# Optimization experiments

Hardware: AMD Instinct MI355X
Metric: run time of the kernel (lower is better)

The kernel has to match this reference:

```python
import jax, jax.numpy as jnp
import numpy as np

NUM_EXPERTS = 8
TOPK = 2
HIDDEN = 2048
INTER = 1024          # intermediate_size_per_rank (world_size = 1)
NTOKENS = 8192        # ntokens; rows of intermediate_states = NTOKENS * TOPK


def setup_inputs() -> dict:
    key = jax.random.key(0)
    k1, k2, k3 = jax.random.split(key, 3)
    intermediate_states = jax.random.normal(k1, (NTOKENS * TOPK, INTER), jnp.float32) * 0.02
    w = jax.random.normal(k2, (NUM_EXPERTS, INTER, HIDDEN), jnp.float32) * 0.02
    router_logits = jax.random.normal(k3, (NTOKENS, NUM_EXPERTS), jnp.float32)
    return {"intermediate_states": intermediate_states, "w": w, "router_logits": router_logits}


def reference(intermediate_states, w, router_logits):
    # select_experts: softmax over experts, then top-k (ids + weights)
    probs = jax.nn.softmax(router_logits, axis=-1)              # [T, E]
    topk_weight, topk_ids = jax.lax.top_k(probs, TOPK)          # [T, K]
    tw = topk_weight.reshape(-1)                                # [T*K]
    tids = topk_ids.reshape(-1)                                 # [T*K]

    # per-expert masked GEMM + router-weight scale (expert loop is a small fixed set)
    out = jnp.zeros((NTOKENS * TOPK, HIDDEN), intermediate_states.dtype)
    for e in range(NUM_EXPERTS):
        mask = (tids == e)[:, None]                             # [T*K, 1]
        xe = jnp.where(mask, intermediate_states, 0.0)          # gather via masking
        out = out + jnp.where(mask, (xe @ w[e]) * tw[:, None], 0.0)

    # sum over topk; reduce_scatter with world_size==1 is the identity
    output = out.reshape(NTOKENS, TOPK, HIDDEN).sum(axis=1)     # [T, H]
    return output
```

## Files before the change

### kernel.cpp

```cpp
#include <hip/hip_runtime.h>
#include <hip/hip_bf16.h>

#define NTOK   8192
#define TOPK   2
#define NROWS  (NTOK*TOPK)
#define NEXP   8
#define KDIM   1024
#define NDIM   2048
#define TM     128
#define TN     128
#define BK     64
#define MAXYT  136
#define NXT    (NDIM/TN)
#define GRID_G (MAXYT*NXT)

typedef __bf16 bf16_t;
typedef __bf16 bf16x8 __attribute__((ext_vector_type(8)));
typedef float  f32x4  __attribute__((ext_vector_type(4)));

static_assert(sizeof(bf16x8) == 16, "bf16x8 must be 16B");

#define OFF_TW    ((size_t)0)
#define OFF_INV   ((size_t)(1<<16))
#define OFF_CNT   ((size_t)(1<<17))
#define OFF_RL    ((size_t)(1<<18))
#define OFF_XP    ((size_t)(1<<20))
#define OFF_WB    ((size_t)(34u<<20))
#define OFF_SCR   ((size_t)(68u<<20))

__device__ __forceinline__ void gload_lds16(const bf16_t* g, const char* l) {
  __builtin_amdgcn_global_load_lds(
      (const __attribute__((address_space(1))) void*)g,
      (__attribute__((address_space(3))) void*)(void*)l, 16, 0, 0);
}

#define CVT8(lo,hi) bf16x8{ (bf16_t)(lo).x,(bf16_t)(lo).y,(bf16_t)(lo).z,(bf16_t)(lo).w, \
                            (bf16_t)(hi).x,(bf16_t)(hi).y,(bf16_t)(hi).z,(bf16_t)(hi).w }

__global__ void routing_kernel(const float* __restrict__ logits,
                               float* __restrict__ tw,
                               int* __restrict__ cnt, int* __restrict__ rowlist) {
  __shared__ int lcnt[NEXP];
  __shared__ int lbase[NEXP];
  int tid = threadIdx.x;
  int t = blockIdx.x * blockDim.x + tid;
  if (tid < NEXP) lcnt[tid] = 0;
  __syncthreads();

  float4 a = *(const float4*)(logits + (size_t)t*NEXP);
  float4 b = *(const float4*)(logits + (size_t)t*NEXP + 4);
  float l[8] = {a.x, a.y, a.z, a.w, b.x, b.y, b.z, b.w};
  float m = l[0];
#pragma unroll
  for (int i = 1; i < 8; i++) m = fmaxf(m, l[i]);
  float p[8], s = 0.f;
#pragma unroll
  for (int i = 0; i < 8; i++) { p[i] = __expf(l[i] - m); s += p[i]; }
  int e0 = 0; float b0 = p[0];
#pragma unroll
  for (int i = 1; i < 8; i++) if (p[i] > b0) { b0 = p[i]; e0 = i; }
  int e1 = (e0 == 0) ? 1 : 0; float b1 = p[e1];
#pragma unroll
  for (int i = 0; i < 8; i++) if (i != e0 && p[i] > b1) { b1 = p[i]; e1 = i; }
  float inv = 1.f / s;
  tw[2*t]   = b0 * inv;
  tw[2*t+1] = b1 * inv;

  int lp0 = atomicAdd(&lcnt[e0], 1);
  int lp1 = atomicAdd(&lcnt[e1], 1);
  __syncthreads();
  if (tid < NEXP) lbase[tid] = atomicAdd(&cnt[tid], lcnt[tid]);
  __syncthreads();
  rowlist[(size_t)e0*NROWS + lbase[e0] + lp0] = 2*t;
  rowlist[(size_t)e1*NROWS + lbase[e1] + lp1] = 2*t + 1;
}

__global__ void cvt_kernel(const float* __restrict__ x,
                           const int* __restrict__ cnt,
                           const int* __restrict__ rowlist,
                           bf16_t* __restrict__ xp,
                           int* __restrict__ inv,
                           const float* __restrict__ w,
                           bf16_t* __restrict__ wb) {
  __shared__ float tf[64*65];
  int bid = blockIdx.x;
  int tid = threadIdx.x;

  if (bid < 2048) {
    int rid = bid * 8 + (tid >> 6);
    int c   = (tid & 63) * 16;
    int e = 0, base = 0, acc = 0;
#pragma unroll
    for (int ee = 0; ee < NEXP; ee++) {
      int ce = cnt[ee];
      if (rid >= acc && rid < acc + ce) { e = ee; base = acc; }
      acc += ce;
    }
    int src = rowlist[(size_t)e*NROWS + (rid - base)];
    const float* sp = x + (size_t)src*KDIM + c;
    float4 v0 = *(const float4*)(sp);
    float4 v1 = *(const float4*)(sp + 4);
    float4 v2 = *(const float4*)(sp + 8);
    float4 v3 = *(const float4*)(sp + 12);
    bf16_t* dp = xp + (size_t)rid*KDIM + c;
    *(bf16x8*)(dp)     = CVT8(v0, v1);
    *(bf16x8*)(dp + 8) = CVT8(v2, v3);
    if ((tid & 63) == 0) inv[src] = rid;
    return;
  }

  int id = bid - 2048;
  int e  = id >> 9;
  int k0 = ((id >> 5) & 15) * 64;
  int n0 = (id & 31) * 64;
  const float* src = w + (size_t)e*KDIM*NDIM + (size_t)k0*NDIM + n0;
#pragma unroll
  for (int i = 0; i < 2; i++) {
    int idx = tid + i*512;
    int kr  = idx >> 4;
    int nc4 = (idx & 15) * 4;
    float4 v = *(const float4*)(src + (size_t)kr*NDIM + nc4);
    tf[kr*65 + nc4+0] = v.x; tf[kr*65 + nc4+1] = v.y;
    tf[kr*65 + nc4+2] = v.z; tf[kr*65 + nc4+3] = v.w;
  }
  __syncthreads();
  bf16_t* dst = wb + (size_t)e*NDIM*KDIM + (size_t)n0*KDIM + k0;
  {
    int idx = tid;
    int nr  = idx >> 3;
    int kc  = (idx & 7) * 8;
    bf16x8 o;
#pragma unroll
    for (int j = 0; j < 8; j++) o[j] = (bf16_t)tf[(kc+j)*65 + nr];
    *(bf16x8*)(dst + (size_t)nr*KDIM + kc) = o;
  }
}

__global__ __launch_bounds__(256)
void gemm_kernel(const bf16_t* __restrict__ xp,
                 const bf16_t* __restrict__ wb,
                 const int*    __restrict__ cnt,
                 bf16_t*       __restrict__ scrb) {
  __shared__ char smem[32768];

  int bid = blockIdx.x;
  int lin = (bid & 7) * (GRID_G/8) + (bid >> 3);
  int xt  = lin & (NXT-1);
  int yt  = lin >> 4;

  int e = -1, rowbase = 0, nrows = 0;
  {
    int a0 = 0, rb = 0;
#pragma unroll
    for (int ee = 0; ee < NEXP; ee++) {
      int c  = cnt[ee];
      int nt = (c + TM - 1) >> 7;
      if (yt >= a0 && yt < a0 + nt) {
        e = ee; rowbase = rb + (yt - a0)*TM;
        nrows = c - (yt - a0)*TM; if (nrows > TM) nrows = TM;
      }
      a0 += nt; rb += c;
    }
  }
  if (e < 0) return;
  const int n0 = xt * TN;

  const int t    = threadIdx.x;
  const int lane = t & 63;
  const int wv   = t >> 6;
  const int wm   = wv >> 1;
  const int wn   = wv & 1;
  const int lr   = lane & 15;
  const int l4   = lane >> 4;

  const int koff = ((t & 7) ^ ((t >> 3) & 7)) * 8;
  int r0 = rowbase + (t >> 3);
  int a0r = r0;      if (a0r > NROWS-1) a0r = NROWS-1;
  int a1r = r0+32;   if (a1r > NROWS-1) a1r = NROWS-1;
  int a2r = r0+64;   if (a2r > NROWS-1) a2r = NROWS-1;
  int a3r = r0+96;   if (a3r > NROWS-1) a3r = NROWS-1;
  const bf16_t* gA0 = xp + (size_t)a0r*KDIM + koff;
  const bf16_t* gA1 = xp + (size_t)a1r*KDIM + koff;
  const bf16_t* gA2 = xp + (size_t)a2r*KDIM + koff;
  const bf16_t* gA3 = xp + (size_t)a3r*KDIM + koff;
  const bf16_t* gBb = wb + ((size_t)e*NDIM + n0 + (t >> 3))*KDIM + koff;
  const char* dA = &smem[t*16];
  const char* dB = &smem[16384 + t*16];

  const int aoff0 = (wm*64 + lr)*128 + ((l4 ^ (lr & 7)) << 4);
  const int boff0 = 16384 + (wn*64 + lr)*128 + ((l4 ^ (lr & 7)) << 4);

  f32x4 acc[4][4] = {};

#pragma unroll 1
  for (int kt = 0; kt < KDIM/BK; ++kt) {
    __syncthreads();
    gload_lds16(gA0, dA);
    gload_lds16(gA1, dA + 4096);
    gload_lds16(gA2, dA + 8192);
    gload_lds16(gA3, dA + 12288);
    gload_lds16(gBb,           dB);
    gload_lds16(gBb + 32*KDIM, dB + 4096);
    gload_lds16(gBb + 64*KDIM, dB + 8192);
    gload_lds16(gBb + 96*KDIM, dB + 12288);
    gA0 += BK; gA1 += BK; gA2 += BK; gA3 += BK; gBb += BK;
    __syncthreads();

    bf16x8 af[4][2], bf[4][2];
#pragma unroll
    for (int mi = 0; mi < 4; mi++) {
      af[mi][0] = *(const bf16x8*)&smem[aoff0 + mi*2048];
      af[mi][1] = *(const bf16x8*)&smem[(aoff0 + mi*2048) ^ 64];
    }
#pragma unroll
    for (int ni = 0; ni < 4; ni++) {
      bf[ni][0] = *(const bf16x8*)&smem[boff0 + ni*2048];
      bf[ni][1] = *(const bf16x8*)&smem[(boff0 + ni*2048) ^ 64];
    }
#pragma unroll
    for (int mi = 0; mi < 4; mi++)
#pragma unroll
      for (int ni = 0; ni < 4; ni++) {
        acc[mi][ni] = __builtin_amdgcn_mfma_f32_16x16x32_bf16(af[mi][0], bf[ni][0], acc[mi][ni], 0, 0, 0);
        acc[mi][ni] = __builtin_amdgcn_mfma_f32_16x16x32_bf16(af[mi][1], bf[ni][1], acc[mi][ni], 0, 0, 0);
      }
  }

#pragma unroll
  for (int mi = 0; mi < 4; mi++) {
#pragma unroll
    for (int jj = 0; jj < 4; jj++) {
      int rbw = wm*64 + mi*16 + l4*4 + jj;
      if (rbw < nrows) {
        bf16_t* dst = scrb + (size_t)(rowbase + rbw)*NDIM + n0 + wn*64 + lr;
#pragma unroll
        for (int ni = 0; ni < 4; ni++) dst[ni*16] = (bf16_t)acc[mi][ni][jj];
      }
    }
  }
}

__global__ void reduce_kernel(const bf16_t* __restrict__ scr,
                              const int* __restrict__ inv,
                              const float* __restrict__ tw,
                              float* __restrict__ out) {
  int g  = blockIdx.x * 512 + threadIdx.x;
  int tk = g >> 7;
  int c  = (g & 127) * 16;
  int2  iv = *(const int2*)(inv + 2*tk);
  float w0 = tw[2*tk], w1 = tw[2*tk+1];
  const bf16_t* pa = scr + (size_t)iv.x*NDIM + c;
  const bf16_t* pb = scr + (size_t)iv.y*NDIM + c;
  bf16x8 a0 = *(const bf16x8*)(pa);
  bf16x8 a1 = *(const bf16x8*)(pa + 8);
  bf16x8 b0 = *(const bf16x8*)(pb);
  bf16x8 b1 = *(const bf16x8*)(pb + 8);
  float* dst = out + (size_t)tk*NDIM + c;
#pragma unroll
  for (int h = 0; h < 2; h++) {
    bf16x8 av = h ? a1 : a0;
    bf16x8 bv = h ? b1 : b0;
    float4 o0 = { w0*(float)av[0]+w1*(float)bv[0], w0*(float)av[1]+w1*(float)bv[1],
                  w0*(float)av[2]+w1*(float)bv[2], w0*(float)av[3]+w1*(float)bv[3] };
    float4 o1 = { w0*(float)av[4]+w1*(float)bv[4], w0*(float)av[5]+w1*(float)bv[5],
                  w0*(float)av[6]+w1*(float)bv[6], w0*(float)av[7]+w1*(float)bv[7] };
    *(float4*)(dst + h*8)     = o0;
    *(float4*)(dst + h*8 + 4) = o1;
  }
}

extern "C" void kernel_launch(void* const* d_in, const int* in_sizes, int n_in,
                              void* d_out, int out_size, void* d_ws, size_t ws_size,
                              hipStream_t stream) {
  const float* x      = (const float*)d_in[0];
  const float* w      = (const float*)d_in[1];
  const float* logits = (const float*)d_in[2];
  float* out = (float*)d_out;

  char* ws = (char*)d_ws;
  float*  tw      = (float*)(ws + OFF_TW);
  int*    inv     = (int*)  (ws + OFF_INV);
  int*    cnt     = (int*)  (ws + OFF_CNT);
  int*    rowlist = (int*)  (ws + OFF_RL);
  bf16_t* xp      = (bf16_t*)(ws + OFF_XP);
  bf16_t* wb      = (bf16_t*)(ws + OFF_WB);
  bf16_t* scrb    = (bf16_t*)(ws + OFF_SCR);

  hipMemsetAsync(cnt, 0, NEXP * sizeof(int), stream);
  routing_kernel<<<NTOK/256, 256, 0, stream>>>(logits, tw, cnt, rowlist);
  cvt_kernel<<<2048 + 4096, 512, 0, stream>>>(x, cnt, rowlist, xp, inv, w, wb);
  gemm_kernel<<<GRID_G, 256, 0, stream>>>(xp, wb, cnt, scrb);
  reduce_kernel<<<NTOK*NDIM/16/512, 512, 0, stream>>>(scrb, inv, tw, out);
}
```

Measured before the change: 157.9 us.

## Pipeline grouped GEMM with 4-stage LDS ring buffer and BK=32

Replaces the single-buffered K loop, which used two block barriers per iteration, with a 4-slot LDS ring of BK=32 stages. Global-to-LDS loads run two stages ahead, with vmcnt waits and one barrier per step. LDS reads use inline ds_read_b128 with immediate offsets, and MFMA issue is wrapped in setprio. LDS grows to 64KB, which may cut occupancy, and the halved K tile doubles the number of loop iterations.

```diff
diff --git a/kernel.cpp b/kernel.cpp
--- a/kernel.cpp
+++ b/kernel.cpp
@@ -9,7 +9,7 @@
 #define NDIM   2048
 #define TM     128
 #define TN     128
-#define BK     64
+#define BK     32
 #define MAXYT  136
 #define NXT    (NDIM/TN)
 #define GRID_G (MAXYT*NXT)
@@ -136,12 +136,45 @@
   }
 }
 
+#define DSREAD(dst, addr, IMM) \
+  asm volatile("ds_read_b128 %0, %1 offset:" #IMM : "=v"(dst) : "v"(addr))
+
+#define STAGE(BI) do {                                                         \
+    const char* dA = smem + (unsigned)(BI)*16384u + t*16;                      \
+    const char* dB = dA + 8192;                                                \
+    gload_lds16(gA0, dA); gload_lds16(gA1, dA + 4096);                         \
+    gload_lds16(gB0, dB); gload_lds16(gB1, dB + 4096);                         \
+    gA0 += BK; gA1 += BK; gB0 += BK; gB1 += BK;                                \
+  } while (0)
+
+#define VMCNT(n) asm volatile("s_waitcnt vmcnt(" #n ")" ::: "memory")
+
+#define COMPUTE(BI) do {                                                       \
+    unsigned ab = sbase + (unsigned)(BI)*16384u + aoff0;                       \
+    unsigned bb = sbase + (unsigned)(BI)*16384u + 8192u + boff0;               \
+    bf16x8 A0,A1,A2,A3,B0,B1,B2,B3;                                            \
+    DSREAD(A0, ab, 0);    DSREAD(A1, ab, 1024);                                \
+    DSREAD(A2, ab, 2048); DSREAD(A3, ab, 3072);                                \
+    DSREAD(B0, bb, 0);    DSREAD(B1, bb, 1024);                                \
+    DSREAD(B2, bb, 2048); DSREAD(B3, bb, 3072);                                \
+    asm volatile("s_waitcnt lgkmcnt(0)" ::: "memory");                         \
+    __builtin_amdgcn_sched_barrier(0);                                         \
+    __builtin_amdgcn_s_setprio(1);                                             \
+    bf16x8 A_[4] = {A0,A1,A2,A3};                                              \
+    bf16x8 B_[4] = {B0,B1,B2,B3};                                              \
+    _Pragma("unroll") for (int mi = 0; mi < 4; mi++)                           \
+      _Pragma("unroll") for (int ni = 0; ni < 4; ni++)                         \
+        acc[mi][ni] = __builtin_amdgcn_mfma_f32_16x16x32_bf16(                 \
+            A_[mi], B_[ni], acc[mi][ni], 0, 0, 0);                             \
+    __builtin_amdgcn_s_setprio(0);                                             \
+  } while (0)
+
 __global__ __launch_bounds__(256)
 void gemm_kernel(const bf16_t* __restrict__ xp,
                  const bf16_t* __restrict__ wb,
                  const int*    __restrict__ cnt,
                  bf16_t*       __restrict__ scrb) {
-  __shared__ char smem[32768];
+  __shared__ char smem[65536];
 
   int bid = blockIdx.x;
   int lin = (bid & 7) * (GRID_G/8) + (bid >> 3);
@@ -173,58 +206,38 @@
   const int lr   = lane & 15;
   const int l4   = lane >> 4;
 
-  const int koff = ((t & 7) ^ ((t >> 3) & 7)) * 8;
-  int r0 = rowbase + (t >> 3);
-  int a0r = r0;      if (a0r > NROWS-1) a0r = NROWS-1;
-  int a1r = r0+32;   if (a1r > NROWS-1) a1r = NROWS-1;
-  int a2r = r0+64;   if (a2r > NROWS-1) a2r = NROWS-1;
-  int a3r = r0+96;   if (a3r > NROWS-1) a3r = NROWS-1;
+  const unsigned sbase = (unsigned)(uintptr_t)
+      (__attribute__((address_space(3))) char*)(void*)smem;
+
+  const int koff = ((t & 3) ^ ((t >> 3) & 3)) * 8;
+  int a0r = rowbase + (t >> 2);       if (a0r > NROWS-1) a0r = NROWS-1;
+  int a1r = rowbase + (t >> 2) + 64;  if (a1r > NROWS-1) a1r = NROWS-1;
   const bf16_t* gA0 = xp + (size_t)a0r*KDIM + koff;
   const bf16_t* gA1 = xp + (size_t)a1r*KDIM + koff;
-  const bf16_t* gA2 = xp + (size_t)a2r*KDIM + koff;
-  const bf16_t* gA3 = xp + (size_t)a3r*KDIM + koff;
-  const bf16_t* gBb = wb + ((size_t)e*NDIM + n0 + (t >> 3))*KDIM + koff;
-  const char* dA = &smem[t*16];
-  const char* dB = &smem[16384 + t*16];
-
-  const int aoff0 = (wm*64 + lr)*128 + ((l4 ^ (lr & 7)) << 4);
-  const int boff0 = 16384 + (wn*64 + lr)*128 + ((l4 ^ (lr & 7)) << 4);
+  const bf16_t* gB0 = wb + ((size_t)e*NDIM + n0 + (t >> 2))*KDIM + koff;
+  const bf16_t* gB1 = gB0 + (size_t)64*KDIM;
+
+  const unsigned aoff0 = (wm*64 + lr)*64 + ((l4 ^ ((lr >> 1) & 3)) << 4);
+  const unsigned boff0 = (wn*64 + lr)*64 + ((l4 ^ ((lr >> 1) & 3)) << 4);
 
   f32x4 acc[4][4] = {};
 
+  STAGE(0);
+  STAGE(1);
+
 #pragma unroll 1
-  for (int kt = 0; kt < KDIM/BK; ++kt) {
-    __syncthreads();
-    gload_lds16(gA0, dA);
-    gload_lds16(gA1, dA + 4096);
-    gload_lds16(gA2, dA + 8192);
-    gload_lds16(gA3, dA + 12288);
-    gload_lds16(gBb,           dB);
-    gload_lds16(gBb + 32*KDIM, dB + 4096);
-    gload_lds16(gBb + 64*KDIM, dB + 8192);
-    gload_lds16(gBb + 96*KDIM, dB + 12288);
-    gA0 += BK; gA1 += BK; gA2 += BK; gA3 += BK; gBb += BK;
-    __syncthreads();
-
-    bf16x8 af[4][2], bf[4][2];
-#pragma unroll
-    for (int mi = 0; mi < 4; mi++) {
-      af[mi][0] = *(const bf16x8*)&smem[aoff0 + mi*2048];
-      af[mi][1] = *(const bf16x8*)&smem[(aoff0 + mi*2048) ^ 64];
-    }
-#pragma unroll
-    for (int ni = 0; ni < 4; ni++) {
-      bf[ni][0] = *(const bf16x8*)&smem[boff0 + ni*2048];
-      bf[ni][1] = *(const bf16x8*)&smem[(boff0 + ni*2048) ^ 64];
-    }
-#pragma unroll
-    for (int mi = 0; mi < 4; mi++)
-#pragma unroll
-      for (int ni = 0; ni < 4; ni++) {
-        acc[mi][ni] = __builtin_amdgcn_mfma_f32_16x16x32_bf16(af[mi][0], bf[ni][0], acc[mi][ni], 0, 0, 0);
-        acc[mi][ni] = __builtin_amdgcn_mfma_f32_16x16x32_bf16(af[mi][1], bf[ni][1], acc[mi][ni], 0, 0, 0);
-      }
-  }
+  for (int kt = 0; kt < 30; ++kt) {
+    STAGE((kt + 2) & 3);
+    VMCNT(8);
+    __builtin_amdgcn_s_barrier();
+    COMPUTE(kt & 3);
+  }
+  VMCNT(4);
+  __builtin_amdgcn_s_barrier();
+  COMPUTE(2);
+  VMCNT(0);
+  __builtin_amdgcn_s_barrier();
+  COMPUTE(3);
 
 #pragma unroll
   for (int mi = 0; mi < 4; mi++) {
```

After: 176.2 us. 11.6% more time.
